# Kernel optimization log

Measured on AMD Instinct MI355X. Metric: run time of the kernel, lower is better.

The kernel has to match this reference:

```python
import jax, jax.numpy as jnp
import numpy as np

B, N, D_IN, D_OUT = 16, 512, 256, 32
C_SP, H, W = 64, 256, 256


def setup_inputs() -> dict:
    key = jax.random.key(0)
    k1, k2, k3, k4, k5 = jax.random.split(key, 5)
    return {
        "spatial_info": jax.random.normal(k1, (B, C_SP, H, W), dtype=jnp.float32),
        "entity_embeddings": jax.random.normal(k2, (B, N, D_IN), dtype=jnp.float32),
        "W_proj": jax.random.normal(k3, (D_IN, D_OUT), dtype=jnp.float32) / np.sqrt(D_IN),
        "b_proj": jax.random.normal(k4, (D_OUT,), dtype=jnp.float32) * 0.01,
        "locations": jax.random.randint(k5, (B, N, 2), 0, 256, dtype=jnp.int32),
    }


def reference(spatial_info, entity_embeddings, W_proj, b_proj, locations):
    # per-entity linear projection (fc_block): [B, N, D_out]
    proj = jnp.einsum('bnd,de->bne', entity_embeddings, W_proj) + b_proj

    Bb, C, Hh, Ww = spatial_info.shape
    # clamp locations like the torch min/max logic
    h = jnp.clip(locations[..., 0], 0, Hh - 1)  # [B, N]
    w = jnp.clip(locations[..., 1], 0, Ww - 1)  # [B, N]
    flat = h * Ww + w                            # [B, N] flattened spatial index

    scatter_map = jnp.zeros((Bb, Hh * Ww, proj.shape[-1]), dtype=spatial_info.dtype)
    b_idx = jnp.arange(Bb, dtype=flat.dtype)[:, None]  # [B, 1]
    scatter_map = scatter_map.at[b_idx, flat].set(proj)
    scatter_map = scatter_map.reshape(Bb, Hh, Ww, -1).transpose(0, 3, 1, 2)  # [B, D_out, H, W]

    return jnp.concatenate([spatial_info, scatter_map], axis=1)
```

## Files before the change

kernel.cpp:

```cpp
#include <hip/hip_runtime.h>

#define BATCH 16
#define NENT  512
#define D_IN  256
#define D_OUT 32
#define CSP   64
#define COUT  96
#define HWDIM 256
#define HWSZ  65536
#define HW4   16384
#define SP_B4  (CSP * HW4)
#define SC_B4  (D_OUT * HW4)
#define OUT_B4 (COUT * HW4)

typedef float vfloat4 __attribute__((ext_vector_type(4)));
typedef int   vint4   __attribute__((ext_vector_type(4)));

__global__ void init_proj_kernel(const float* __restrict__ emb,
                                 const float* __restrict__ Wp,
                                 const float* __restrict__ bp,
                                 vint4* __restrict__ owner4,
                                 float* __restrict__ projbuf) {
    int tid = blockIdx.x * blockDim.x + threadIdx.x;
    const int NZ4 = BATCH * HWSZ / 4;
    if (tid < NZ4) {
        vint4 z = {0, 0, 0, 0};
        owner4[tid] = z;
        return;
    }
    int gid = tid - NZ4;
    int ent = gid >> 5;
    int e   = gid & 31;
    const vfloat4* er4 = (const vfloat4*)(emb + (size_t)ent * D_IN);
    float acc = bp[e];
    #pragma unroll 8
    for (int d4 = 0; d4 < D_IN / 4; ++d4) {
        vfloat4 ev = er4[d4];
        int d = d4 * 4;
        acc += ev.x * Wp[(d + 0) * D_OUT + e];
        acc += ev.y * Wp[(d + 1) * D_OUT + e];
        acc += ev.z * Wp[(d + 2) * D_OUT + e];
        acc += ev.w * Wp[(d + 3) * D_OUT + e];
    }
    projbuf[gid] = acc;
}

__global__ void owner_kernel(const int* __restrict__ loc,
                             int* __restrict__ owner) {
    int gid = blockIdx.x * blockDim.x + threadIdx.x;
    if (gid >= BATCH * NENT) return;
    int h = min(max(loc[gid * 2 + 0], 0), HWDIM - 1);
    int w = min(max(loc[gid * 2 + 1], 0), HWDIM - 1);
    int b = gid >> 9;
    int n = gid & (NENT - 1);
    atomicMax(&owner[b * HWSZ + h * HWDIM + w], n + 1);
}

__global__ void fused_out_kernel(const vfloat4* __restrict__ sp,
                                 const vint4* __restrict__ owner4,
                                 const float* __restrict__ projbuf,
                                 vfloat4* __restrict__ out) {
    const int PER = 2048 * 256;
    int b = blockIdx.y;
    int t = blockIdx.x * blockDim.x + threadIdx.x;

    const vfloat4* spb  = sp  + (size_t)b * SP_B4;
    vfloat4*       outb = out + (size_t)b * OUT_B4;

    vfloat4 c0 = __builtin_nontemporal_load(&spb[t]);
    __builtin_nontemporal_store(c0, &outb[t]);
    vfloat4 c1 = __builtin_nontemporal_load(&spb[t + PER]);
    __builtin_nontemporal_store(c1, &outb[t + PER]);

    int e   = t >> 14;
    int hw4 = t & (HW4 - 1);
    vint4 ow = owner4[b * HW4 + hw4];
    const float* pb = projbuf + b * (NENT * D_OUT) + e;
    float vx = pb[max(ow.x - 1, 0) * D_OUT];
    float vy = pb[max(ow.y - 1, 0) * D_OUT];
    float vz = pb[max(ow.z - 1, 0) * D_OUT];
    float vw = pb[max(ow.w - 1, 0) * D_OUT];
    vfloat4 v;
    v.x = ow.x ? vx : 0.f;
    v.y = ow.y ? vy : 0.f;
    v.z = ow.z ? vz : 0.f;
    v.w = ow.w ? vw : 0.f;
    __builtin_nontemporal_store(v, &outb[SP_B4 + t]);
}

extern "C" void kernel_launch(void* const* d_in, const int* in_sizes, int n_in,
                              void* d_out, int out_size, void* d_ws, size_t ws_size,
                              hipStream_t stream) {
    const float* spatial = (const float*)d_in[0];
    const float* emb     = (const float*)d_in[1];
    const float* Wp      = (const float*)d_in[2];
    const float* bp      = (const float*)d_in[3];
    const int*   loc     = (const int*)d_in[4];
    float* out = (float*)d_out;

    int*   owner   = (int*)d_ws;
    float* projbuf = (float*)((char*)d_ws + BATCH * HWSZ * sizeof(int));

    init_proj_kernel<<<2048, 256, 0, stream>>>(emb, Wp, bp, (vint4*)owner, projbuf);
    owner_kernel<<<32, 256, 0, stream>>>(loc, owner);
    dim3 grid(2048, BATCH);
    fused_out_kernel<<<grid, 256, 0, stream>>>((const vfloat4*)spatial,
                                               (const vint4*)owner, projbuf,
                                               (vfloat4*)out);
}
```

Measured before the change: 137.1 us.

## Merge owner scatter into prologue and split output into copy and fill kernels

Owner-map zeroing and the atomicMax scatter now run in one prologue kernel, with one 512-thread block per batch that zeros its slice, synchronizes, then scatters. Projection blocks run in the same launch, so the separate owner kernel is gone. The fused output kernel is split into a pure streaming copy kernel and a separate gather/fill kernel, which separates the bandwidth-bound copy from the dependent gather loads. The risks are that only 16 blocks now zero the 4 MB owner map, and that the copy and gather no longer overlap within one kernel.

Result: faster. 134.2 us (-2.1%).

```diff
diff --git a/kernel.cpp b/kernel.cpp
--- a/kernel.cpp
+++ b/kernel.cpp
@@ -12,23 +12,35 @@
 #define SP_B4  (CSP * HW4)
 #define SC_B4  (D_OUT * HW4)
 #define OUT_B4 (COUT * HW4)
+#define PER    (2048 * 256)
 
 typedef float vfloat4 __attribute__((ext_vector_type(4)));
 typedef int   vint4   __attribute__((ext_vector_type(4)));
 
-__global__ void init_proj_kernel(const float* __restrict__ emb,
-                                 const float* __restrict__ Wp,
-                                 const float* __restrict__ bp,
-                                 vint4* __restrict__ owner4,
-                                 float* __restrict__ projbuf) {
-    int tid = blockIdx.x * blockDim.x + threadIdx.x;
-    const int NZ4 = BATCH * HWSZ / 4;
-    if (tid < NZ4) {
+__global__ __launch_bounds__(512)
+void prologue_kernel(const float* __restrict__ emb,
+                     const float* __restrict__ Wp,
+                     const float* __restrict__ bp,
+                     const int* __restrict__ loc,
+                     int* __restrict__ owner,
+                     float* __restrict__ projbuf) {
+    int bid = blockIdx.x;
+    int tid = threadIdx.x;
+    if (bid < BATCH) {
+        vint4* ow4 = (vint4*)(owner + bid * HWSZ);
         vint4 z = {0, 0, 0, 0};
-        owner4[tid] = z;
+        #pragma unroll
+        for (int k = 0; k < 32; ++k) {
+            ow4[tid + k * 512] = z;
+        }
+        __syncthreads();
+        int ent = bid * NENT + tid;
+        int h = min(max(loc[ent * 2 + 0], 0), HWDIM - 1);
+        int w = min(max(loc[ent * 2 + 1], 0), HWDIM - 1);
+        atomicMax(&owner[bid * HWSZ + h * HWDIM + w], tid + 1);
         return;
     }
-    int gid = tid - NZ4;
+    int gid = (bid - BATCH) * 512 + tid;
     int ent = gid >> 5;
     int e   = gid & 31;
     const vfloat4* er4 = (const vfloat4*)(emb + (size_t)ent * D_IN);
@@ -45,33 +57,25 @@
     projbuf[gid] = acc;
 }
 
-__global__ void owner_kernel(const int* __restrict__ loc,
-                             int* __restrict__ owner) {
-    int gid = blockIdx.x * blockDim.x + threadIdx.x;
-    if (gid >= BATCH * NENT) return;
-    int h = min(max(loc[gid * 2 + 0], 0), HWDIM - 1);
-    int w = min(max(loc[gid * 2 + 1], 0), HWDIM - 1);
-    int b = gid >> 9;
-    int n = gid & (NENT - 1);
-    atomicMax(&owner[b * HWSZ + h * HWDIM + w], n + 1);
-}
-
-__global__ void fused_out_kernel(const vfloat4* __restrict__ sp,
-                                 const vint4* __restrict__ owner4,
-                                 const float* __restrict__ projbuf,
-                                 vfloat4* __restrict__ out) {
-    const int PER = 2048 * 256;
+__global__ __launch_bounds__(256)
+void copy_kernel(const vfloat4* __restrict__ sp,
+                 vfloat4* __restrict__ out) {
     int b = blockIdx.y;
     int t = blockIdx.x * blockDim.x + threadIdx.x;
-
     const vfloat4* spb  = sp  + (size_t)b * SP_B4;
     vfloat4*       outb = out + (size_t)b * OUT_B4;
-
     vfloat4 c0 = __builtin_nontemporal_load(&spb[t]);
     __builtin_nontemporal_store(c0, &outb[t]);
     vfloat4 c1 = __builtin_nontemporal_load(&spb[t + PER]);
     __builtin_nontemporal_store(c1, &outb[t + PER]);
+}
 
+__global__ __launch_bounds__(256)
+void fill_kernel(const vint4* __restrict__ owner4,
+                 const float* __restrict__ projbuf,
+                 vfloat4* __restrict__ out) {
+    int b = blockIdx.y;
+    int t = blockIdx.x * blockDim.x + threadIdx.x;
     int e   = t >> 14;
     int hw4 = t & (HW4 - 1);
     vint4 ow = owner4[b * HW4 + hw4];
@@ -85,7 +89,7 @@
     v.y = ow.y ? vy : 0.f;
     v.z = ow.z ? vz : 0.f;
     v.w = ow.w ? vw : 0.f;
-    __builtin_nontemporal_store(v, &outb[SP_B4 + t]);
+    __builtin_nontemporal_store(v, &out[(size_t)b * OUT_B4 + SP_B4 + t]);
 }
 
 extern "C" void kernel_launch(void* const* d_in, const int* in_sizes, int n_in,
@@ -101,10 +105,11 @@
     int*   owner   = (int*)d_ws;
     float* projbuf = (float*)((char*)d_ws + BATCH * HWSZ * sizeof(int));
 
-    init_proj_kernel<<<2048, 256, 0, stream>>>(emb, Wp, bp, (vint4*)owner, projbuf);
-    owner_kernel<<<32, 256, 0, stream>>>(loc, owner);
+    prologue_kernel<<<BATCH + 512, 512, 0, stream>>>(emb, Wp, bp, loc,
+                                                     owner, projbuf);
     dim3 grid(2048, BATCH);
-    fused_out_kernel<<<grid, 256, 0, stream>>>((const vfloat4*)spatial,
-                                               (const vint4*)owner, projbuf,
-                                               (vfloat4*)out);
+    copy_kernel<<<grid, 256, 0, stream>>>((const vfloat4*)spatial,
+                                          (vfloat4*)out);
+    fill_kernel<<<grid, 256, 0, stream>>>((const vint4*)owner, projbuf,
+                                          (vfloat4*)out);
 }
```
